# Optimization experiments

Hardware: AMD Instinct MI355X
Metric: run time of the kernel (lower is better)

Reference implementation:

```python
import jax, jax.numpy as jnp
import numpy as np

NEG_INF = -1.0e7


def positional_encodings(max_seq_len, hidden_size):
    pos = jnp.arange(max_seq_len, dtype=jnp.float32)[:, None]
    dim = jnp.arange(hidden_size // 2, dtype=jnp.float32)[None, :]
    args = pos / (10000.0 ** (2.0 * dim / hidden_size))  # (max_seq_len, h/2)
    pe = jnp.zeros((max_seq_len, hidden_size), dtype=jnp.float32)
    pe = pe.at[:, 0::2].set(jnp.sin(args)).at[:, 1::2].set(jnp.cos(args))
    return pe


def _attention(x_q, x_kv, Wq, bq, Wk, bk, Wv, bv, scale, causal):
    # Linear layers (torch Linear: y = x @ W^T + b; here W stored as (in, out)).
    q = x_q @ Wq + bq            # (B, Sq, H)
    k = x_kv @ Wk + bk           # (B, Sk, H)
    v = x_kv @ Wv + bv           # (B, Sk, H)
    scores = jnp.einsum('bqh,bkh->bqk', q, k) * scale  # (B, Sq, Sk)
    if causal:
        sq, sk = scores.shape[1], scores.shape[2]
        # original adds neg_inf * tril(ones, diag=-1) on (B, Sk, Sq): masked when k_idx > q_idx
        mask = (jnp.arange(sk)[None, :] > jnp.arange(sq)[:, None]).astype(scores.dtype)
        scores = scores + NEG_INF * mask
    w = jax.nn.softmax(scores, axis=-1)                # (B, Sq, Sk)
    ctx = jnp.einsum('bqk,bkh->bqh', w, v)
    return ctx, jnp.transpose(w, (0, 2, 1))            # weights returned as (B, Sk, Sq)


def setup_inputs() -> dict:
    B, S_dec, S_enc, H, V, L = 8, 512, 512, 1024, 32000, 6
    key = jax.random.key(0)
    ks = jax.random.split(key, 20)
    s = 0.02
    inp = {
        'inputs': jax.random.randint(ks[0], (B, S_dec), 0, V),
        'annotations': jax.random.normal(ks[1], (B, S_enc, H), dtype=jnp.float32),
        'hidden_init': jnp.zeros((B, H), dtype=jnp.float32),
        'embedding': jax.random.normal(ks[2], (V, H), dtype=jnp.float32) * s,
        'Wq_s': jax.random.normal(ks[3], (L, H, H), dtype=jnp.float32) * s,
        'bq_s': jnp.zeros((L, H), dtype=jnp.float32),
        'Wk_s': jax.random.normal(ks[4], (L, H, H), dtype=jnp.float32) * s,
        'bk_s': jnp.zeros((L, H), dtype=jnp.float32),
        'Wv_s': jax.random.normal(ks[5], (L, H, H), dtype=jnp.float32) * s,
        'bv_s': jnp.zeros((L, H), dtype=jnp.float32),
        'Wq_c': jax.random.normal(ks[6], (L, H, H), dtype=jnp.float32) * s,
        'bq_c': jnp.zeros((L, H), dtype=jnp.float32),
        'Wk_c': jax.random.normal(ks[7], (L, H, H), dtype=jnp.float32) * s,
        'bk_c': jnp.zeros((L, H), dtype=jnp.float32),
        'Wv_c': jax.random.normal(ks[8], (L, H, H), dtype=jnp.float32) * s,
        'bv_c': jnp.zeros((L, H), dtype=jnp.float32),
        'Wm': jax.random.normal(ks[9], (L, H, H), dtype=jnp.float32) * s,
        'bm': jnp.zeros((L, H), dtype=jnp.float32),
        'Wout': jax.random.normal(ks[10], (H, V), dtype=jnp.float32) * s,
        'bout': jnp.zeros((V,), dtype=jnp.float32),
    }
    return inp


def reference(inputs, annotations, hidden_init, embedding,
              Wq_s, bq_s, Wk_s, bk_s, Wv_s, bv_s,
              Wq_c, bq_c, Wk_c, bk_c, Wv_c, bv_c,
              Wm, bm, Wout, bout):
    B, S = inputs.shape
    L, H, _ = Wq_s.shape
    scale = 1.0 / jnp.sqrt(jnp.asarray(H, dtype=jnp.float32))
    pe = positional_encodings(1000, H)
    contexts = embedding[inputs] + pe[:S]              # (B, S, H)
    enc_ws, self_ws = [], []
    for i in range(L):
        new_ctx, sw = _attention(contexts, contexts,
                                 Wq_s[i], bq_s[i], Wk_s[i], bk_s[i], Wv_s[i], bv_s[i],
                                 scale, causal=True)
        residual = contexts + new_ctx
        new_ctx, ew = _attention(residual, annotations,
                                 Wq_c[i], bq_c[i], Wk_c[i], bk_c[i], Wv_c[i], bv_c[i],
                                 scale, causal=False)
        residual = residual + new_ctx
        mlp = jax.nn.relu(residual @ Wm[i] + bm[i])
        contexts = residual + mlp
        enc_ws.append(ew)
        self_ws.append(sw)
    output = contexts @ Wout + bout                    # (B, S, V)
    return output, (jnp.stack(enc_ws), jnp.stack(self_ws))
```

## Files before the change

kernel.cpp:

```cpp
#include <hip/hip_runtime.h>

typedef __attribute__((ext_vector_type(4))) float f4;
typedef __attribute__((ext_vector_type(8))) short s8v;
typedef __attribute__((ext_vector_type(4))) short s4v;

__device__ __forceinline__ short f2bf(float f) {
  union { float f; unsigned int u; } v; v.f = f;
  unsigned int u = v.u;
  unsigned int r = 0x7fffu + ((u >> 16) & 1u);
  return (short)((u + r) >> 16);
}

__device__ __forceinline__ void glds16(const void* g, void* l) {
  __builtin_amdgcn_global_load_lds((const __attribute__((address_space(1))) void*)g,
                                   (__attribute__((address_space(3))) void*)l, 16, 0, 0);
}

template<int BIAS, int RES, int RELU, int OF32, int OBF>
__global__ __launch_bounds__(256) void gemmp(
    const unsigned short* __restrict__ A, const unsigned short* __restrict__ Bt,
    const float* __restrict__ bias, const float* __restrict__ bias2,
    const float* __restrict__ res,
    float* __restrict__ Cf, unsigned short* __restrict__ Cb,
    int lda, int ldb, int ldc, int ldcb, int ldr, int nk,
    long sA, long sB, long sC, long sCb, long sR, long sBias) {
  __shared__ __align__(1024) char lds[98304];
  int tid = threadIdx.x;
  int bx = blockIdx.x, by = blockIdx.y, bz = blockIdx.z;
  int bm0 = by * 128, bn0 = bx * 128;
  const char* Ag = (const char*)(A + bz * sA);
  const char* Bg = (const char*)(Bt + bz * sB);
  if (BIAS) { bias += bz * sBias; if (BIAS == 3) bias2 += bz * sBias; }
  int w = tid >> 6, lane = tid & 63;
  int sr = tid >> 3;
  int skb = ((tid & 7) ^ (sr & 7)) << 4;
  size_t la2 = (size_t)lda * 2, lb2 = (size_t)ldb * 2;
  char* bf0 = lds;
  char* bf1 = lds + 32768;
  char* bf2 = lds + 65536;
  int wm = (w >> 1) * 64, wn = (w & 1) * 64;
  int rb = lane & 15;
  int kx = (lane & 7) << 4;
  int kb0 = (lane >> 4) << 4;
  f4 acc[4][4] = {};

  auto stageH = [&](char* buf, int kt, int h) {
    size_t ka = (size_t)kt * 128 + skb;
    if (h == 0) {
      glds16(Ag + (size_t)(bm0 + sr) * la2 + ka,            buf + w * 1024);
      glds16(Ag + (size_t)(bm0 + 32 + sr) * la2 + ka,       buf + 4096 + w * 1024);
      glds16(Bg + (size_t)(bn0 + sr) * lb2 + ka,            buf + 16384 + w * 1024);
      glds16(Bg + (size_t)(bn0 + 32 + sr) * lb2 + ka,       buf + 20480 + w * 1024);
    } else {
      glds16(Ag + (size_t)(bm0 + 64 + sr) * la2 + ka,       buf + 8192 + w * 1024);
      glds16(Ag + (size_t)(bm0 + 96 + sr) * la2 + ka,       buf + 12288 + w * 1024);
      glds16(Bg + (size_t)(bn0 + 64 + sr) * lb2 + ka,       buf + 24576 + w * 1024);
      glds16(Bg + (size_t)(bn0 + 96 + sr) * lb2 + ka,       buf + 28672 + w * 1024);
    }
  };
  auto phase = [&](const char* buf, int ks) {
    const char* Ar = buf + (wm + rb) * 128;
    const char* Br = buf + 16384 + (wn + rb) * 128;
    int kb = (kb0 + ks * 64) ^ kx;
    s8v a[4], b[4];
#pragma unroll
    for (int i = 0; i < 4; ++i) a[i] = *(const s8v*)(Ar + i * 2048 + kb);
#pragma unroll
    for (int j = 0; j < 4; ++j) b[j] = *(const s8v*)(Br + j * 2048 + kb);
    __builtin_amdgcn_s_setprio(1);
#pragma unroll
    for (int i = 0; i < 4; ++i)
#pragma unroll
      for (int j = 0; j < 4; ++j)
        acc[i][j] = __builtin_amdgcn_mfma_f32_16x16x32_bf16(b[j], a[i], acc[i][j], 0, 0, 0);
    __builtin_amdgcn_s_setprio(0);
  };

  stageH(bf0, 0, 0); stageH(bf0, 0, 1);
  stageH(bf1, 1, 0); stageH(bf1, 1, 1);

  for (int t = 0; t < nk - 2; ++t) {
    stageH(bf2, t + 2, 0);
    asm volatile("s_waitcnt vmcnt(12)" ::: "memory");
    __builtin_amdgcn_s_barrier();
    __builtin_amdgcn_sched_barrier(0);
    phase(bf0, 0);
    __builtin_amdgcn_s_barrier();
    stageH(bf2, t + 2, 1);
    __builtin_amdgcn_s_barrier();
    __builtin_amdgcn_sched_barrier(0);
    phase(bf0, 1);
    __builtin_amdgcn_s_barrier();
    char* tp = bf0; bf0 = bf1; bf1 = bf2; bf2 = tp;
  }
  asm volatile("s_waitcnt vmcnt(8)" ::: "memory");
  __builtin_amdgcn_s_barrier();
  __builtin_amdgcn_sched_barrier(0);
  phase(bf0, 0);
  __builtin_amdgcn_s_barrier();
  __builtin_amdgcn_sched_barrier(0);
  phase(bf0, 1);
  __builtin_amdgcn_s_barrier();
  asm volatile("s_waitcnt vmcnt(0)" ::: "memory");
  __builtin_amdgcn_s_barrier();
  __builtin_amdgcn_sched_barrier(0);
  phase(bf1, 0);
  phase(bf1, 1);

  float* Cfp = Cf + bz * sC;
  unsigned short* Cbp = Cb + bz * sCb;
  const float* Rp = res + bz * sR;
  float* E = (float*)lds;
  __syncthreads();
#pragma unroll
  for (int i = 0; i < 4; ++i) {
    int lr = wm + i * 16 + (lane & 15);
    int sw = (lr & 7) << 2;
#pragma unroll
    for (int j = 0; j < 4; ++j) {
      int col = wn + j * 16 + ((lane >> 4) << 2);
      *(f4*)&E[lr * 128 + (col ^ sw)] = acc[i][j];
    }
  }
  __syncthreads();
#pragma unroll
  for (int p = 0; p < 16; ++p) {
    int fi = p * 256 + tid;
    int row = fi >> 5, c4 = fi & 31;
    f4 v = *(const f4*)&E[row * 128 + ((c4 ^ (row & 7)) << 2)];
    int rr = bm0 + row;
    int col = bn0 + c4 * 4;
    if (BIAS == 1) { v[0] += bias[col]; v[1] += bias[col+1]; v[2] += bias[col+2]; v[3] += bias[col+3]; }
    if (BIAS == 2) { float bb = bias[rr]; v[0] += bb; v[1] += bb; v[2] += bb; v[3] += bb; }
    if (BIAS == 3) {
      const float* bp = (col < 1024) ? (bias + col) : (bias2 + (col - 1024));
      v[0] += bp[0]; v[1] += bp[1]; v[2] += bp[2]; v[3] += bp[3];
    }
    if (RELU) { v[0]=fmaxf(v[0],0.f); v[1]=fmaxf(v[1],0.f); v[2]=fmaxf(v[2],0.f); v[3]=fmaxf(v[3],0.f); }
    if (RES) { f4 rv = *(const f4*)(Rp + (size_t)rr * ldr + col); v[0]+=rv[0]; v[1]+=rv[1]; v[2]+=rv[2]; v[3]+=rv[3]; }
    if (OF32) *(f4*)(Cfp + (size_t)rr * ldc + col) = v;
    if (OBF) {
      s4v o; o[0]=f2bf(v[0]); o[1]=f2bf(v[1]); o[2]=f2bf(v[2]); o[3]=f2bf(v[3]);
      *(s4v*)(Cbp + (size_t)rr * ldcb + col) = o;
    }
  }
}

template<int RES, int OF32, int OBF>
__global__ __launch_bounds__(256) void gemm64(
    const unsigned short* __restrict__ A, const unsigned short* __restrict__ Bt,
    const float* __restrict__ res,
    float* __restrict__ Cf, unsigned short* __restrict__ Cb,
    int lda, int ldb, int ldc, int ldcb, int ldr, int nk,
    long sA, long sB, long sC, long sCb, long sR) {
  __shared__ __align__(16) char smem[16384];
  int tid = threadIdx.x;
  int bx = blockIdx.x, by = blockIdx.y, bz = blockIdx.z;
  int bm0 = by * 64, bn0 = bx * 64;
  const char* Ag = (const char*)(A + bz * sA);
  const char* Bg = (const char*)(Bt + bz * sB);
  int w = tid >> 6, lane = tid & 63;
  int sr = tid >> 3;
  int skb = ((tid & 7) ^ (sr & 7)) << 4;
  size_t la2 = (size_t)lda * 2, lb2 = (size_t)ldb * 2;
  char* Al = smem + w * 1024;
  char* Bl = smem + 8192 + w * 1024;
  int wm = (w >> 1) * 32, wn = (w & 1) * 32;
  int rb = lane & 15;
  int kx = (lane & 7) << 4;
  int kb0 = (lane >> 4) << 4;
  const char* Ar = smem + (wm + rb) * 128;
  const char* Br = smem + 8192 + (wn + rb) * 128;
  f4 acc[2][2] = {};
  for (int kt = 0; kt < nk; ++kt) {
    size_t ka = (size_t)kt * 128 + skb;
    __syncthreads();
#pragma unroll
    for (int p = 0; p < 2; ++p)
      glds16(Ag + (size_t)(bm0 + p * 32 + sr) * la2 + ka, Al + p * 4096);
#pragma unroll
    for (int p = 0; p < 2; ++p)
      glds16(Bg + (size_t)(bn0 + p * 32 + sr) * lb2 + ka, Bl + p * 4096);
    __syncthreads();
#pragma unroll
    for (int ks = 0; ks < 2; ++ks) {
      int kb = (kb0 + ks * 64) ^ kx;
      s8v a[2], b[2];
#pragma unroll
      for (int i = 0; i < 2; ++i) a[i] = *(const s8v*)(Ar + i * 2048 + kb);
#pragma unroll
      for (int j = 0; j < 2; ++j) b[j] = *(const s8v*)(Br + j * 2048 + kb);
#pragma unroll
      for (int i = 0; i < 2; ++i)
#pragma unroll
        for (int j = 0; j < 2; ++j)
          acc[i][j] = __builtin_amdgcn_mfma_f32_16x16x32_bf16(b[j], a[i], acc[i][j], 0, 0, 0);
    }
  }
  float* Cfp = Cf + bz * sC;
  unsigned short* Cbp = Cb + bz * sCb;
  const float* Rp = res + bz * sR;
  float* E = (float*)smem;
  __syncthreads();
#pragma unroll
  for (int i = 0; i < 2; ++i) {
    int lr = wm + i * 16 + (lane & 15);
    int sw = (lr & 7) << 2;
#pragma unroll
    for (int j = 0; j < 2; ++j) {
      int col = wn + j * 16 + ((lane >> 4) << 2);
      *(f4*)&E[lr * 64 + (col ^ sw)] = acc[i][j];
    }
  }
  __syncthreads();
#pragma unroll
  for (int p = 0; p < 4; ++p) {
    int fi = p * 256 + tid;
    int row = fi >> 4, c4 = fi & 15;
    f4 v = *(const f4*)&E[row * 64 + ((c4 ^ (row & 7)) << 2)];
    int rr = bm0 + row;
    int col = bn0 + c4 * 4;
    if (RES) { f4 rv = *(const f4*)(Rp + (size_t)rr * ldr + col); v[0]+=rv[0]; v[1]+=rv[1]; v[2]+=rv[2]; v[3]+=rv[3]; }
    if (OF32) *(f4*)(Cfp + (size_t)rr * ldc + col) = v;
    if (OBF) {
      s4v o; o[0]=f2bf(v[0]); o[1]=f2bf(v[1]); o[2]=f2bf(v[2]); o[3]=f2bf(v[3]);
      *(s4v*)(Cbp + (size_t)rr * ldcb + col) = o;
    }
  }
}

__global__ __launch_bounds__(512) void gemm_logits(
    const unsigned short* __restrict__ A, const unsigned short* __restrict__ Bt,
    const float* __restrict__ bias, float* __restrict__ C) {
  __shared__ __align__(1024) char lds[147456];
  const int ldc = 32000, nk = 16;
  int tid = threadIdx.x;
  int w = tid >> 6, lane = tid & 63;
  int id = blockIdx.y * 250 + blockIdx.x;
  int nid = (id & 7) * 500 + (id >> 3);
  int bx = nid % 250, by = nid / 250;
  int bm0 = by * 256, bn0 = bx * 128;
  const size_t ld2 = 2048;
  const char* Ag = (const char*)A;
  const char* Bg = (const char*)Bt;
  int srow = (w << 3) + (lane >> 3);
  size_t ska = (size_t)(((lane & 7) ^ (lane >> 3)) << 4);
  char* bf0 = lds;
  char* bf1 = lds + 49152;
  char* bf2 = lds + 98304;
  int wm = (w >> 1) * 64;
  int wn = (w & 1) * 64;
  int rsel = lane & 15;
  int kx = (lane & 7) << 4;
  int kb0 = (lane >> 4) << 4;
  f4 acc[4][4] = {};

  auto stageH = [&](char* buf, int kt, int h) {
    size_t ka = (size_t)kt * 128 + ska;
    if (h == 0) {
      glds16(Ag + (size_t)(bm0 + srow) * ld2 + ka,       buf + w * 1024);
      glds16(Ag + (size_t)(bm0 + 64 + srow) * ld2 + ka,  buf + 8192 + w * 1024);
      glds16(Bg + (size_t)(bn0 + srow) * ld2 + ka,       buf + 32768 + w * 1024);
    } else {
      glds16(Ag + (size_t)(bm0 + 128 + srow) * ld2 + ka, buf + 16384 + w * 1024);
      glds16(Ag + (size_t)(bm0 + 192 + srow) * ld2 + ka, buf + 24576 + w * 1024);
      glds16(Bg + (size_t)(bn0 + 64 + srow) * ld2 + ka,  buf + 40960 + w * 1024);
    }
  };
  auto phase = [&](const char* buf, int ks) {
    const char* Ab = buf + (wm + rsel) * 128;
    const char* Bb = buf + 32768 + (wn + rsel) * 128;
    int kb = (kb0 + ks * 64) ^ kx;
    s8v a0 = *(const s8v*)(Ab + kb);
    s8v a1 = *(const s8v*)(Ab + 2048 + kb);
    s8v a2 = *(const s8v*)(Ab + 4096 + kb);
    s8v a3 = *(const s8v*)(Ab + 6144 + kb);
    s8v q0 = *(const s8v*)(Bb + kb);
    s8v q1 = *(const s8v*)(Bb + 2048 + kb);
    s8v q2 = *(const s8v*)(Bb + 4096 + kb);
    s8v q3 = *(const s8v*)(Bb + 6144 + kb);
    __builtin_amdgcn_s_setprio(1);
    acc[0][0] = __builtin_amdgcn_mfma_f32_16x16x32_bf16(q0, a0, acc[0][0], 0, 0, 0);
    acc[0][1] = __builtin_amdgcn_mfma_f32_16x16x32_bf16(q1, a0, acc[0][1], 0, 0, 0);
    acc[0][2] = __builtin_amdgcn_mfma_f32_16x16x32_bf16(q2, a0, acc[0][2], 0, 0, 0);
    acc[0][3] = __builtin_amdgcn_mfma_f32_16x16x32_bf16(q3, a0, acc[0][3], 0, 0, 0);
    acc[1][0] = __builtin_amdgcn_mfma_f32_16x16x32_bf16(q0, a1, acc[1][0], 0, 0, 0);
    acc[1][1] = __builtin_amdgcn_mfma_f32_16x16x32_bf16(q1, a1, acc[1][1], 0, 0, 0);
    acc[1][2] = __builtin_amdgcn_mfma_f32_16x16x32_bf16(q2, a1, acc[1][2], 0, 0, 0);
    acc[1][3] = __builtin_amdgcn_mfma_f32_16x16x32_bf16(q3, a1, acc[1][3], 0, 0, 0);
    acc[2][0] = __builtin_amdgcn_mfma_f32_16x16x32_bf16(q0, a2, acc[2][0], 0, 0, 0);
    acc[2][1] = __builtin_amdgcn_mfma_f32_16x16x32_bf16(q1, a2, acc[2][1], 0, 0, 0);
    acc[2][2] = __builtin_amdgcn_mfma_f32_16x16x32_bf16(q2, a2, acc[2][2], 0, 0, 0);
    acc[2][3] = __builtin_amdgcn_mfma_f32_16x16x32_bf16(q3, a2, acc[2][3], 0, 0, 0);
    acc[3][0] = __builtin_amdgcn_mfma_f32_16x16x32_bf16(q0, a3, acc[3][0], 0, 0, 0);
    acc[3][1] = __builtin_amdgcn_mfma_f32_16x16x32_bf16(q1, a3, acc[3][1], 0, 0, 0);
    acc[3][2] = __builtin_amdgcn_mfma_f32_16x16x32_bf16(q2, a3, acc[3][2], 0, 0, 0);
    acc[3][3] = __builtin_amdgcn_mfma_f32_16x16x32_bf16(q3, a3, acc[3][3], 0, 0, 0);
    __builtin_amdgcn_s_setprio(0);
  };

  stageH(bf0, 0, 0); stageH(bf0, 0, 1);
  stageH(bf1, 1, 0); stageH(bf1, 1, 1);

  for (int t = 0; t < nk - 2; ++t) {
    stageH(bf2, t + 2, 0);
    asm volatile("s_waitcnt vmcnt(9)" ::: "memory");
    __builtin_amdgcn_s_barrier();
    __builtin_amdgcn_sched_barrier(0);
    phase(bf0, 0);
    __builtin_amdgcn_s_barrier();
    stageH(bf2, t + 2, 1);
    __builtin_amdgcn_s_barrier();
    __builtin_amdgcn_sched_barrier(0);
    phase(bf0, 1);
    __builtin_amdgcn_s_barrier();
    char* tp = bf0; bf0 = bf1; bf1 = bf2; bf2 = tp;
  }
  asm volatile("s_waitcnt vmcnt(6)" ::: "memory");
  __builtin_amdgcn_s_barrier();
  __builtin_amdgcn_sched_barrier(0);
  phase(bf0, 0);
  __builtin_amdgcn_s_barrier();
  __builtin_amdgcn_sched_barrier(0);
  phase(bf0, 1);
  __builtin_amdgcn_s_barrier();
  asm volatile("s_waitcnt vmcnt(0)" ::: "memory");
  __builtin_amdgcn_s_barrier();
  __builtin_amdgcn_sched_barrier(0);
  phase(bf1, 0);
  phase(bf1, 1);

  float* E = (float*)lds;
  __syncthreads();
#pragma unroll
  for (int i = 0; i < 4; ++i) {
    int lr = wm + i * 16 + (lane & 15);
    int sw = (lr & 7) << 2;
#pragma unroll
    for (int j = 0; j < 4; ++j) {
      int col = wn + j * 16 + ((lane >> 4) << 2);
      *(f4*)&E[lr * 128 + (col ^ sw)] = acc[i][j];
    }
  }
  __syncthreads();
#pragma unroll
  for (int p = 0; p < 16; ++p) {
    int fi = p * 512 + tid;
    int row = fi >> 5, c4 = fi & 31;
    f4 v = *(const f4*)&E[row * 128 + ((c4 ^ (row & 7)) << 2)];
    int rr = bm0 + row;
    int col = bn0 + c4 * 4;
    v[0] += bias[col]; v[1] += bias[col+1]; v[2] += bias[col+2]; v[3] += bias[col+3];
    __builtin_nontemporal_store(v, (f4*)(C + (size_t)rr * ldc + col));
  }
}

__device__ __forceinline__ void wtrans_tile(const float* src, unsigned short* dst,
                                            int rows, int cols, int c0, int r0) {
  __shared__ float t[64][65];
  int tx = threadIdx.x & 63, ty = threadIdx.x >> 6;
#pragma unroll
  for (int j = 0; j < 16; ++j) {
    int r = j * 4 + ty;
    t[r][tx] = src[(size_t)(r0 + r) * cols + c0 + tx];
  }
  __syncthreads();
#pragma unroll
  for (int j = 0; j < 16; ++j) {
    int n = j * 4 + ty;
    dst[(size_t)(c0 + n) * rows + r0 + tx] = (unsigned short)f2bf(t[tx][n]);
  }
}

__global__ __launch_bounds__(256) void wtrans_k(const float* __restrict__ src,
                                                unsigned short* __restrict__ dst,
                                                int rows, int cols) {
  wtrans_tile(src, dst, rows, cols, blockIdx.x * 64, blockIdx.y * 64);
}

__global__ __launch_bounds__(256) void wtrans_all_k(
    const float* __restrict__ w0, const float* __restrict__ w1,
    const float* __restrict__ w2, const float* __restrict__ w3,
    const float* __restrict__ w4, const float* __restrict__ w5,
    const float* __restrict__ w6, unsigned short* __restrict__ dst) {
  int z = blockIdx.z;
  int l = z / 7, wi = z % 7;
  const float* src;
  switch (wi) {
    case 0: src = w0; break;
    case 1: src = w1; break;
    case 2: src = w2; break;
    case 3: src = w3; break;
    case 4: src = w4; break;
    case 5: src = w5; break;
    default: src = w6; break;
  }
  src += (size_t)l * 1024 * 1024;
  unsigned short* d = dst + (size_t)z * 1024 * 1024;
  wtrans_tile(src, d, 1024, 1024, blockIdx.x * 64, blockIdx.y * 64);
}

__global__ __launch_bounds__(256) void convbf_k(const float* __restrict__ src,
                                                unsigned short* __restrict__ dst, int n4) {
  int i = blockIdx.x * 256 + threadIdx.x;
  if (i >= n4) return;
  f4 f = ((const f4*)src)[i];
  s4v v;
  v[0] = f2bf(f[0]); v[1] = f2bf(f[1]); v[2] = f2bf(f[2]); v[3] = f2bf(f[3]);
  ((s4v*)dst)[i] = v;
}

template<int CAUSAL>
__global__ __launch_bounds__(512) void smt_k(const float* __restrict__ Sf,
                                             float* __restrict__ outT,
                                             unsigned short* __restrict__ Wb) {
  __shared__ float T[32][524];
  int b = blockIdx.y;
  int q0 = blockIdx.x * 32;
  int t = threadIdx.x;
  const float* Sp = Sf + ((size_t)b * 512 + q0) * 512;
#pragma unroll
  for (int j = 0; j < 8; ++j) {
    int idx = t + 512 * j;
    int r = idx >> 7, c4 = idx & 127;
    f4 v = *(const f4*)(Sp + (size_t)r * 512 + c4 * 4);
    *(f4*)&T[r][c4 * 4] = v;
  }
  __syncthreads();
  int w = t >> 6, l = t & 63;
  int r = 4 * w + (l >> 4);
  int l16 = l & 15;
  int q = q0 + r;
  const float scale = 0.03125f;
  float v[32];
#pragma unroll
  for (int j = 0; j < 32; ++j) {
    int k = l16 + 16 * j;
    float x = T[r][k] * scale;
    if (CAUSAL && k > q) x += -1.0e7f;
    v[j] = x;
  }
  float m = v[0];
#pragma unroll
  for (int j = 1; j < 32; ++j) m = fmaxf(m, v[j]);
  m = fmaxf(m, __shfl_xor(m, 1)); m = fmaxf(m, __shfl_xor(m, 2));
  m = fmaxf(m, __shfl_xor(m, 4)); m = fmaxf(m, __shfl_xor(m, 8));
  float s = 0.f;
#pragma unroll
  for (int j = 0; j < 32; ++j) { v[j] = __expf(v[j] - m); s += v[j]; }
  s += __shfl_xor(s, 1); s += __shfl_xor(s, 2);
  s += __shfl_xor(s, 4); s += __shfl_xor(s, 8);
  float inv = 1.0f / s;
#pragma unroll
  for (int j = 0; j < 32; ++j) T[r][l16 + 16 * j] = v[j] * inv;
  __syncthreads();
  float* op = outT + (size_t)b * 512 * 512 + q0;
  int ql = t & 31, kb = t >> 5;
#pragma unroll
  for (int i = 0; i < 32; ++i) {
    int k = kb + 16 * i;
    __builtin_nontemporal_store(T[ql][k], &op[(size_t)k * 512 + ql]);
  }
  unsigned short* wp = Wb + ((size_t)b * 512 + q0) * 512;
#pragma unroll
  for (int i = 0; i < 4; ++i) {
    int rr = 4 * w + i;
    const float* row = &T[rr][l * 8];
    s8v o;
#pragma unroll
    for (int j = 0; j < 8; ++j) o[j] = f2bf(row[j]);
    *(s8v*)(wp + (size_t)rr * 512 + l * 8) = o;
  }
}

__global__ __launch_bounds__(256) void embed_pe_k(const int* __restrict__ ids,
                                                  const float* __restrict__ emb,
                                                  float* __restrict__ ctx,
                                                  unsigned short* __restrict__ ctxb) {
  int row = blockIdx.x;
  int s = row & 511;
  int t = threadIdx.x;
  int id = ids[row];
  f4 e = *(const f4*)(emb + (size_t)id * 1024 + t * 4);
  int j0 = 2 * t, j1 = 2 * t + 1;
  float fr0 = powf(10000.0f, -2.0f * (float)j0 / 1024.0f);
  float fr1 = powf(10000.0f, -2.0f * (float)j1 / 1024.0f);
  float s0, c0, s1, c1;
  sincosf((float)s * fr0, &s0, &c0);
  sincosf((float)s * fr1, &s1, &c1);
  f4 o;
  o[0] = e[0] + s0; o[1] = e[1] + c0; o[2] = e[2] + s1; o[3] = e[3] + c1;
  *(f4*)(ctx + (size_t)row * 1024 + t * 4) = o;
  s4v ob;
  ob[0] = f2bf(o[0]); ob[1] = f2bf(o[1]); ob[2] = f2bf(o[2]); ob[3] = f2bf(o[3]);
  *(s4v*)(ctxb + (size_t)row * 1024 + t * 4) = ob;
}

extern "C" void kernel_launch(void* const* d_in, const int* in_sizes, int n_in,
                              void* d_out, int out_size, void* d_ws, size_t ws_size,
                              hipStream_t stream) {
  const int B = 8, S = 512, H = 1024, V = 32000, L = 6;
  const int M = B * S;

  const int* ids = (const int*)d_in[0];
  const float* ann = (const float*)d_in[1];
  const float* emb = (const float*)d_in[3];
  const float* bq_s = (const float*)d_in[5];
  const float* bk_s = (const float*)d_in[7];
  const float* bv_s = (const float*)d_in[9];
  const float* bq_c = (const float*)d_in[11];
  const float* bk_c = (const float*)d_in[13];
  const float* bv_c = (const float*)d_in[15];
  const float* bm = (const float*)d_in[17];
  const float* Wout = (const float*)d_in[18];
  const float* bout = (const float*)d_in[19];
  float* out = (float*)d_out;

  char* ws = (char*)d_ws;
  if (ws_size < ((size_t)164 << 20)) return;
  float* X0 = (float*)ws;
  unsigned short* Xs0 = (unsigned short*)(ws + ((size_t)16 << 20));
  unsigned short* Xs1 = (unsigned short*)(ws + ((size_t)24 << 20));
  unsigned short* QKbf = (unsigned short*)(ws + ((size_t)32 << 20));
  unsigned short* Vtbf = (unsigned short*)(ws + ((size_t)48 << 20));
  float* Sbuf = (float*)(ws + ((size_t)56 << 20));
  unsigned short* Wbf = (unsigned short*)(ws + ((size_t)64 << 20));
  unsigned short* annbf = (unsigned short*)(ws + ((size_t)68 << 20));
  unsigned short* WT = (unsigned short*)(ws + ((size_t)76 << 20));
  unsigned short* KcAll = (unsigned short*)d_out;
  unsigned short* VtcAll = (unsigned short*)((char*)d_out + ((size_t)48 << 20));

  size_t enc_off = (size_t)M * V;
  size_t self_off = enc_off + (size_t)L * B * S * S;

  long sQ = (long)S * H;
  long sS = (long)S * S;
  const size_t WSZ = (size_t)H * H;
  const long sW7 = (long)(7 * WSZ);

  embed_pe_k<<<M, 256, 0, stream>>>(ids, emb, X0, Xs0);
  convbf_k<<<(M * H / 4 + 255) / 256, 256, 0, stream>>>(ann, annbf, M * H / 4);
  wtrans_all_k<<<dim3(16, 16, 42), 256, 0, stream>>>(
      (const float*)d_in[4], (const float*)d_in[6], (const float*)d_in[8],
      (const float*)d_in[10], (const float*)d_in[12], (const float*)d_in[14],
      (const float*)d_in[16], WT);
  gemmp<1, 0, 0, 0, 1><<<dim3(8, 32, 6), 256, 0, stream>>>(
      annbf, WT + 4 * WSZ, bk_c, nullptr, nullptr, nullptr, KcAll,
      H, H, 0, H, 0, 16, 0, sW7, 0, (long)M * H, 0, H);
  gemmp<2, 0, 0, 0, 1><<<dim3(32, 8, 6), 256, 0, stream>>>(
      WT + 5 * WSZ, annbf, bv_c, nullptr, nullptr, nullptr, VtcAll,
      H, H, 0, M, 0, 16, sW7, 0, 0, (long)H * M, 0, H);

  unsigned short* Xa = Xs0;
  unsigned short* Xb = Xs1;

  for (int l = 0; l < L; ++l) {
    size_t bo = (size_t)l * H;
    unsigned short* WTl = WT + (size_t)l * 7 * WSZ;

    gemmp<3, 0, 0, 0, 1><<<dim3(16, 32), 256, 0, stream>>>(
        Xa, WTl, bq_s + bo, bk_s + bo, nullptr, nullptr, QKbf,
        H, H, 0, 2048, 0, 16, 0, 0, 0, 0, 0, 0);
    gemmp<2, 0, 0, 0, 1><<<dim3(32, 8), 256, 0, stream>>>(
        WTl + 2 * WSZ, Xa, bv_s + bo, nullptr, nullptr, nullptr, Vtbf,
        H, H, 0, M, 0, 16, 0, 0, 0, 0, 0, 0);
    gemm64<0, 1, 0><<<dim3(8, 8, B), 256, 0, stream>>>(
        QKbf, QKbf + 1024, nullptr, Sbuf, nullptr,
        2048, 2048, S, 0, 0, 16, (long)S * 2048, (long)S * 2048, sS, 0, 0);
    smt_k<1><<<dim3(16, B), 512, 0, stream>>>(
        Sbuf, out + self_off + (size_t)l * B * S * S, Wbf);
    gemm64<1, 1, 1><<<dim3(16, 8, B), 256, 0, stream>>>(
        Wbf, Vtbf, X0, X0, Xb,
        S, M, H, H, H, 8, sS, 512, sQ, sQ, sQ);
    gemmp<1, 0, 0, 0, 1><<<dim3(8, 32), 256, 0, stream>>>(
        Xb, WTl + 3 * WSZ, bq_c + bo, nullptr, nullptr, nullptr, QKbf,
        H, H, 0, 1024, 0, 16, 0, 0, 0, 0, 0, 0);
    gemm64<0, 1, 0><<<dim3(8, 8, B), 256, 0, stream>>>(
        QKbf, KcAll + (size_t)l * M * H, nullptr, Sbuf, nullptr,
        1024, 1024, S, 0, 0, 16, (long)S * 1024, (long)S * 1024, sS, 0, 0);
    smt_k<0><<<dim3(16, B), 512, 0, stream>>>(
        Sbuf, out + enc_off + (size_t)l * B * S * S, Wbf);
    gemm64<1, 1, 1><<<dim3(16, 8, B), 256, 0, stream>>>(
        Wbf, VtcAll + (size_t)l * H * M, X0, X0, Xa,
        S, M, H, H, H, 8, sS, 512, sQ, sQ, sQ);
    gemmp<1, 1, 1, 1, 1><<<dim3(8, 32), 256, 0, stream>>>(
        Xa, WTl + 6 * WSZ, bm + bo, nullptr, X0, X0, Xb,
        H, H, H, H, H, 16, 0, 0, 0, 0, 0, 0);
    unsigned short* tb = Xa; Xa = Xb; Xb = tb;
  }

  wtrans_k<<<dim3(V / 64, H / 64), 256, 0, stream>>>(Wout, WT, H, V);
  gemm_logits<<<dim3(250, 16), 512, 0, stream>>>(Xa, WT, bout, out);
}
```

Before: 1.473 ms.

## Fuse QKV and cross K/V projections into single GEMMs with transposed V epilogue

Merges the per-layer self-attention Q/K projection and the separate V-transpose projection into one wider GEMM launch, with a new epilogue that writes the V columns transposed through LDS. Does the same for the precomputed cross-attention K and V over all layers. Biases are concatenated once by a new small kernel. Also changes the block-to-tile mapping in the logits GEMM for different cache locality. This cuts launches and fills the GPU better, at the cost of a strided transposed store path and a little extra setup.

```diff
diff --git a/kernel.cpp b/kernel.cpp
--- a/kernel.cpp
+++ b/kernel.cpp
@@ -16,21 +16,22 @@
                                    (__attribute__((address_space(3))) void*)l, 16, 0, 0);
 }
 
-template<int BIAS, int RES, int RELU, int OF32, int OBF>
+template<int BIAS, int RES, int RELU, int OF32, int OBF, int VT>
 __global__ __launch_bounds__(256) void gemmp(
     const unsigned short* __restrict__ A, const unsigned short* __restrict__ Bt,
     const float* __restrict__ bias, const float* __restrict__ bias2,
     const float* __restrict__ res,
     float* __restrict__ Cf, unsigned short* __restrict__ Cb,
+    unsigned short* __restrict__ Cvt, int vtoff, int ldvt,
     int lda, int ldb, int ldc, int ldcb, int ldr, int nk,
-    long sA, long sB, long sC, long sCb, long sR, long sBias) {
+    long sA, long sB, long sC, long sCb, long sR, long sBias, long sVt) {
   __shared__ __align__(1024) char lds[98304];
   int tid = threadIdx.x;
   int bx = blockIdx.x, by = blockIdx.y, bz = blockIdx.z;
   int bm0 = by * 128, bn0 = bx * 128;
   const char* Ag = (const char*)(A + bz * sA);
   const char* Bg = (const char*)(Bt + bz * sB);
-  if (BIAS) { bias += bz * sBias; if (BIAS == 3) bias2 += bz * sBias; }
+  if (BIAS) bias += bz * sBias;
   int w = tid >> 6, lane = tid & 63;
   int sr = tid >> 3;
   int skb = ((tid & 7) ^ (sr & 7)) << 4;
@@ -107,9 +108,6 @@
   phase(bf1, 0);
   phase(bf1, 1);
 
-  float* Cfp = Cf + bz * sC;
-  unsigned short* Cbp = Cb + bz * sCb;
-  const float* Rp = res + bz * sR;
   float* E = (float*)lds;
   __syncthreads();
 #pragma unroll
@@ -123,25 +121,43 @@
     }
   }
   __syncthreads();
-#pragma unroll
-  for (int p = 0; p < 16; ++p) {
-    int fi = p * 256 + tid;
-    int row = fi >> 5, c4 = fi & 31;
-    f4 v = *(const f4*)&E[row * 128 + ((c4 ^ (row & 7)) << 2)];
-    int rr = bm0 + row;
-    int col = bn0 + c4 * 4;
-    if (BIAS == 1) { v[0] += bias[col]; v[1] += bias[col+1]; v[2] += bias[col+2]; v[3] += bias[col+3]; }
-    if (BIAS == 2) { float bb = bias[rr]; v[0] += bb; v[1] += bb; v[2] += bb; v[3] += bb; }
-    if (BIAS == 3) {
-      const float* bp = (col < 1024) ? (bias + col) : (bias2 + (col - 1024));
-      v[0] += bp[0]; v[1] += bp[1]; v[2] += bp[2]; v[3] += bp[3];
-    }
-    if (RELU) { v[0]=fmaxf(v[0],0.f); v[1]=fmaxf(v[1],0.f); v[2]=fmaxf(v[2],0.f); v[3]=fmaxf(v[3],0.f); }
-    if (RES) { f4 rv = *(const f4*)(Rp + (size_t)rr * ldr + col); v[0]+=rv[0]; v[1]+=rv[1]; v[2]+=rv[2]; v[3]+=rv[3]; }
-    if (OF32) *(f4*)(Cfp + (size_t)rr * ldc + col) = v;
-    if (OBF) {
-      s4v o; o[0]=f2bf(v[0]); o[1]=f2bf(v[1]); o[2]=f2bf(v[2]); o[3]=f2bf(v[3]);
-      *(s4v*)(Cbp + (size_t)rr * ldcb + col) = o;
+  if (VT && bn0 >= vtoff) {
+    unsigned short* Vp = Cvt + bz * sVt;
+    int hb = bn0 - vtoff;
+#pragma unroll
+    for (int p = 0; p < 16; ++p) {
+      int fi = p * 256 + tid;
+      int m4 = (fi & 31) * 4, h = fi >> 5;
+      float bb = (BIAS == 1) ? bias[bn0 + h] : 0.f;
+      s4v o;
+#pragma unroll
+      for (int i = 0; i < 4; ++i) {
+        int m = m4 + i;
+        float x = E[m * 128 + (h ^ ((m & 7) << 2))] + bb;
+        o[i] = f2bf(x);
+      }
+      *(s4v*)(Vp + (size_t)(hb + h) * ldvt + bm0 + m4) = o;
+    }
+  } else {
+    float* Cfp = Cf + bz * sC;
+    unsigned short* Cbp = Cb + bz * sCb;
+    const float* Rp = res + bz * sR;
+#pragma unroll
+    for (int p = 0; p < 16; ++p) {
+      int fi = p * 256 + tid;
+      int row = fi >> 5, c4 = fi & 31;
+      f4 v = *(const f4*)&E[row * 128 + ((c4 ^ (row & 7)) << 2)];
+      int rr = bm0 + row;
+      int col = bn0 + c4 * 4;
+      if (BIAS == 1) { v[0] += bias[col]; v[1] += bias[col+1]; v[2] += bias[col+2]; v[3] += bias[col+3]; }
+      if (BIAS == 2) { float bb = bias[rr]; v[0] += bb; v[1] += bb; v[2] += bb; v[3] += bb; }
+      if (RELU) { v[0]=fmaxf(v[0],0.f); v[1]=fmaxf(v[1],0.f); v[2]=fmaxf(v[2],0.f); v[3]=fmaxf(v[3],0.f); }
+      if (RES) { f4 rv = *(const f4*)(Rp + (size_t)rr * ldr + col); v[0]+=rv[0]; v[1]+=rv[1]; v[2]+=rv[2]; v[3]+=rv[3]; }
+      if (OF32) *(f4*)(Cfp + (size_t)rr * ldc + col) = v;
+      if (OBF) {
+        s4v o; o[0]=f2bf(v[0]); o[1]=f2bf(v[1]); o[2]=f2bf(v[2]); o[3]=f2bf(v[3]);
+        *(s4v*)(Cbp + (size_t)rr * ldcb + col) = o;
+      }
     }
   }
 }
@@ -237,8 +253,9 @@
   int tid = threadIdx.x;
   int w = tid >> 6, lane = tid & 63;
   int id = blockIdx.y * 250 + blockIdx.x;
-  int nid = (id & 7) * 500 + (id >> 3);
-  int bx = nid % 250, by = nid / 250;
+  int k = id & 7, j = id >> 3;
+  int by = ((k >> 1) << 2) + (j & 3);
+  int bx = (k & 1) * 125 + (j >> 2);
   int bm0 = by * 256, bn0 = bx * 128;
   const size_t ld2 = 2048;
   const char* Ag = (const char*)A;
@@ -410,6 +427,20 @@
   ((s4v*)dst)[i] = v;
 }
 
+__global__ __launch_bounds__(1024) void catb_k(
+    const float* __restrict__ bq, const float* __restrict__ bk,
+    const float* __restrict__ bv, const float* __restrict__ bkc,
+    const float* __restrict__ bvc, float* __restrict__ catb,
+    float* __restrict__ catbc) {
+  int l = blockIdx.x, t = threadIdx.x;
+  size_t o = (size_t)l * 1024 + t;
+  catb[(size_t)l * 3072 + t] = bq[o];
+  catb[(size_t)l * 3072 + 1024 + t] = bk[o];
+  catb[(size_t)l * 3072 + 2048 + t] = bv[o];
+  catbc[(size_t)l * 2048 + t] = bkc[o];
+  catbc[(size_t)l * 2048 + 1024 + t] = bvc[o];
+}
+
 template<int CAUSAL>
 __global__ __launch_bounds__(512) void smt_k(const float* __restrict__ Sf,
                                              float* __restrict__ outT,
@@ -527,6 +558,8 @@
   unsigned short* Wbf = (unsigned short*)(ws + ((size_t)64 << 20));
   unsigned short* annbf = (unsigned short*)(ws + ((size_t)68 << 20));
   unsigned short* WT = (unsigned short*)(ws + ((size_t)76 << 20));
+  float* catb = (float*)(ws + ((size_t)160 << 20));
+  float* catbc = (float*)(ws + ((size_t)160 << 20) + (96 << 10));
   unsigned short* KcAll = (unsigned short*)d_out;
   unsigned short* VtcAll = (unsigned short*)((char*)d_out + ((size_t)48 << 20));
 
@@ -540,16 +573,16 @@
 
   embed_pe_k<<<M, 256, 0, stream>>>(ids, emb, X0, Xs0);
   convbf_k<<<(M * H / 4 + 255) / 256, 256, 0, stream>>>(ann, annbf, M * H / 4);
+  catb_k<<<L, 1024, 0, stream>>>(bq_s, bk_s, bv_s, bk_c, bv_c, catb, catbc);
   wtrans_all_k<<<dim3(16, 16, 42), 256, 0, stream>>>(
       (const float*)d_in[4], (const float*)d_in[6], (const float*)d_in[8],
       (const float*)d_in[10], (const float*)d_in[12], (const float*)d_in[14],
       (const float*)d_in[16], WT);
-  gemmp<1, 0, 0, 0, 1><<<dim3(8, 32, 6), 256, 0, stream>>>(
-      annbf, WT + 4 * WSZ, bk_c, nullptr, nullptr, nullptr, KcAll,
-      H, H, 0, H, 0, 16, 0, sW7, 0, (long)M * H, 0, H);
-  gemmp<2, 0, 0, 0, 1><<<dim3(32, 8, 6), 256, 0, stream>>>(
-      WT + 5 * WSZ, annbf, bv_c, nullptr, nullptr, nullptr, VtcAll,
-      H, H, 0, M, 0, 16, sW7, 0, 0, (long)H * M, 0, H);
+  gemmp<1, 0, 0, 0, 1, 1><<<dim3(16, 32, 6), 256, 0, stream>>>(
+      annbf, WT + 4 * WSZ, catbc, nullptr, nullptr,
+      nullptr, KcAll, VtcAll, 1024, M,
+      H, H, 0, H, 0, 16,
+      0, sW7, 0, (long)M * H, 0, 2048, (long)H * M);
 
   unsigned short* Xa = Xs0;
   unsigned short* Xb = Xs1;
@@ -558,12 +591,11 @@
     size_t bo = (size_t)l * H;
     unsigned short* WTl = WT + (size_t)l * 7 * WSZ;
 
-    gemmp<3, 0, 0, 0, 1><<<dim3(16, 32), 256, 0, stream>>>(
-        Xa, WTl, bq_s + bo, bk_s + bo, nullptr, nullptr, QKbf,
-        H, H, 0, 2048, 0, 16, 0, 0, 0, 0, 0, 0);
-    gemmp<2, 0, 0, 0, 1><<<dim3(32, 8), 256, 0, stream>>>(
-        WTl + 2 * WSZ, Xa, bv_s + bo, nullptr, nullptr, nullptr, Vtbf,
-        H, H, 0, M, 0, 16, 0, 0, 0, 0, 0, 0);
+    gemmp<1, 0, 0, 0, 1, 1><<<dim3(24, 32), 256, 0, stream>>>(
+        Xa, WTl, catb + (size_t)l * 3072, nullptr, nullptr,
+        nullptr, QKbf, Vtbf, 2048, M,
+        H, H, 0, 2048, 0, 16,
+        0, 0, 0, 0, 0, 0, 0);
     gemm64<0, 1, 0><<<dim3(8, 8, B), 256, 0, stream>>>(
         QKbf, QKbf + 1024, nullptr, Sbuf, nullptr,
         2048, 2048, S, 0, 0, 16, (long)S * 2048, (long)S * 2048, sS, 0, 0);
@@ -572,9 +604,11 @@
     gemm64<1, 1, 1><<<dim3(16, 8, B), 256, 0, stream>>>(
         Wbf, Vtbf, X0, X0, Xb,
         S, M, H, H, H, 8, sS, 512, sQ, sQ, sQ);
-    gemmp<1, 0, 0, 0, 1><<<dim3(8, 32), 256, 0, stream>>>(
-        Xb, WTl + 3 * WSZ, bq_c + bo, nullptr, nullptr, nullptr, QKbf,
-        H, H, 0, 1024, 0, 16, 0, 0, 0, 0, 0, 0);
+    gemmp<1, 0, 0, 0, 1, 0><<<dim3(8, 32), 256, 0, stream>>>(
+        Xb, WTl + 3 * WSZ, bq_c + bo, nullptr, nullptr,
+        nullptr, QKbf, nullptr, 0, 0,
+        H, H, 0, 1024, 0, 16,
+        0, 0, 0, 0, 0, 0, 0);
     gemm64<0, 1, 0><<<dim3(8, 8, B), 256, 0, stream>>>(
         QKbf, KcAll + (size_t)l * M * H, nullptr, Sbuf, nullptr,
         1024, 1024, S, 0, 0, 16, (long)S * 1024, (long)S * 1024, sS, 0, 0);
@@ -583,9 +617,11 @@
     gemm64<1, 1, 1><<<dim3(16, 8, B), 256, 0, stream>>>(
         Wbf, VtcAll + (size_t)l * H * M, X0, X0, Xa,
         S, M, H, H, H, 8, sS, 512, sQ, sQ, sQ);
-    gemmp<1, 1, 1, 1, 1><<<dim3(8, 32), 256, 0, stream>>>(
-        Xa, WTl + 6 * WSZ, bm + bo, nullptr, X0, X0, Xb,
-        H, H, H, H, H, 16, 0, 0, 0, 0, 0, 0);
+    gemmp<1, 1, 1, 1, 1, 0><<<dim3(8, 32), 256, 0, stream>>>(
+        Xa, WTl + 6 * WSZ, bm + bo, nullptr, X0,
+        X0, Xb, nullptr, 0, 0,
+        H, H, H, H, H, 16,
+        0, 0, 0, 0, 0, 0, 0);
     unsigned short* tb = Xa; Xa = Xb; Xb = tb;
   }
 
```

After: 1.508 ms. 2.4% more time.
